# Optimization experiments

Hardware: AMD Instinct MI355X
Metric: run time of the kernel (lower is better)

Reference implementation:

```python
import jax, jax.numpy as jnp
import numpy as np

B, D, H, DH = 2048, 1024, 8, 64  # batch, query_dim, heads, dim_head
INNER = H * DH  # 512


def setup_inputs() -> dict:
    key = jax.random.key(0)
    k0, k1, k2, k3 = jax.random.split(key, 4)
    x = jax.random.normal(k0, (B, D), dtype=jnp.float32)
    Wq = jax.random.normal(k1, (D, INNER), dtype=jnp.float32) * 0.02
    Wkv = jax.random.normal(k2, (D, 2 * INNER), dtype=jnp.float32) * 0.02
    Wout = jax.random.normal(k3, (INNER, D), dtype=jnp.float32) * 0.02
    bout = jnp.zeros((D,), dtype=jnp.float32)
    return {"x": x, "Wq": Wq, "Wkv": Wkv, "Wout": Wout, "bout": bout}


def reference(x, Wq, Wkv, Wout, bout):
    # Faithful to the original: 2D x, attention over the flattened (B*H) axis.
    b = x.shape[0]
    scale = DH ** -0.5
    q = (x @ Wq).reshape(b * H, DH)            # (b h) d
    k, v = jnp.split(x @ Wkv, 2, axis=-1)      # each [b, inner]
    k = k.reshape(b * H, DH)
    v = v.reshape(b * H, DH)
    sim = (q @ k.T) * scale                    # [(b h), (b h)] -- 1 GB intermediate
    attn = jax.nn.softmax(sim, axis=-1)        # dropout_rate = 0 -> identity
    out = (attn @ v).reshape(b, INNER)         # b (h d)
    return out @ Wout + bout                   # project_out path
```

## Files before the change

kernel.cpp:

```cpp
#include <hip/hip_runtime.h>
#include <hip/hip_bf16.h>
#include <stdint.h>


typedef __bf16 bf16_t;
typedef __bf16 bf16x4 __attribute__((ext_vector_type(4)));
typedef __bf16 bf16x8 __attribute__((ext_vector_type(8)));
typedef float floatx4 __attribute__((ext_vector_type(4)));

__device__ __forceinline__ floatx4 mfma16(bf16x8 a, bf16x8 b, floatx4 c) {
    return __builtin_amdgcn_mfma_f32_16x16x32_bf16(a, b, c, 0, 0, 0);
}

__device__ __forceinline__ bf16x8 cvt8(float4 a, float4 b) {
    bf16x8 o;
    o[0] = (bf16_t)a.x; o[1] = (bf16_t)a.y; o[2] = (bf16_t)a.z; o[3] = (bf16_t)a.w;
    o[4] = (bf16_t)b.x; o[5] = (bf16_t)b.y; o[6] = (bf16_t)b.z; o[7] = (bf16_t)b.w;
    return o;
}

__device__ __forceinline__ void transpose_body(const float* __restrict__ in, int N,
                                               bf16_t* __restrict__ out, int ldo,
                                               int bx, int by, int tid, float (*tile)[33]) {
    int n0 = bx * 32, k0 = by * 32;
    int tx = tid & 31, ty = tid >> 5;
#pragma unroll
    for (int i = 0; i < 32; i += 8)
        tile[ty + i][tx] = in[(size_t)(k0 + ty + i) * N + (n0 + tx)];
    __syncthreads();
#pragma unroll
    for (int i = 0; i < 32; i += 8)
        out[(size_t)(n0 + ty + i) * ldo + (k0 + tx)] = (bf16_t)tile[tx][ty + i];
}

__global__ __launch_bounds__(256) void prep_all(const float* __restrict__ x,
                                                bf16_t* __restrict__ xb,
                                                const float* __restrict__ Wq,
                                                const float* __restrict__ Wkv,
                                                const float* __restrict__ Wout,
                                                bf16_t* __restrict__ WtQKV,
                                                bf16_t* __restrict__ WtOut) {
    __shared__ float tile[32][33];
    int b = blockIdx.x, tid = threadIdx.x;
    if (b < 1024) {
        int i = (b * 256 + tid) * 8;
        *(bf16x8*)(xb + i) = cvt8(*(const float4*)(x + i), *(const float4*)(x + i + 4));
    } else if (b < 1536) {
        b -= 1024;
        transpose_body(Wq, 512, WtQKV, 1024, b & 15, b >> 4, tid, tile);
    } else if (b < 2560) {
        b -= 1536;
        transpose_body(Wkv, 1024, WtQKV + 512 * 1024, 1024, b & 31, b >> 5, tid, tile);
    } else {
        b -= 2560;
        transpose_body(Wout, 1024, WtOut, 512, b & 31, b >> 5, tid, tile);
    }
}

template <int OF32, int MI>
__global__ __launch_bounds__(256) void gemm_bt(const bf16_t* __restrict__ A,
                                               const bf16_t* __restrict__ Bt,
                                               const float* __restrict__ bias,
                                               void* __restrict__ Cout,
                                               bf16_t* __restrict__ VtOut, int vt_col0,
                                               int K, int lda, int ldb, int ldc,
                                               float qscale, int qcols) {
    constexpr int MT = MI * 32;
    constexpr int PA = MT / 64;
    constexpr int ABUF = MT * 64;
    __shared__ bf16_t sA[2 * ABUF];
    __shared__ bf16_t sB[2 * 4096];
    int tid = threadIdx.x;
    int wave = tid >> 6, lane = tid & 63;
    int lm = lane & 15, q = lane >> 4;
    int bm = blockIdx.x * MT, bn = blockIdx.y * 64;
    int wm = (wave >> 1) * (MT / 2), wn = (wave & 1) * 32;

    int c0 = (tid & 3) * 2, c1 = c0 + 1;
    int rA[PA], swA[PA];
    size_t srcA0[PA], srcA1[PA];
#pragma unroll
    for (int p = 0; p < PA; ++p) {
        rA[p] = p * 64 + (tid >> 2);
        swA[p] = rA[p] & 7;
        srcA0[p] = (size_t)(bm + rA[p]) * lda + ((c0 ^ swA[p]) << 3);
        srcA1[p] = (size_t)(bm + rA[p]) * lda + ((c1 ^ swA[p]) << 3);
    }
    int rB = tid >> 2, swB = rB & 7;
    size_t srcB0 = (size_t)(bn + rB) * ldb + ((c0 ^ swB) << 3);
    size_t srcB1 = (size_t)(bn + rB) * ldb + ((c1 ^ swB) << 3);

    floatx4 acc[MI][2];
#pragma unroll
    for (int i = 0; i < MI; ++i)
#pragma unroll
        for (int j = 0; j < 2; ++j) acc[i][j] = (floatx4){0.f, 0.f, 0.f, 0.f};

    bf16x8 pa0[PA], pa1[PA], pb0, pb1;
#pragma unroll
    for (int p = 0; p < PA; ++p) {
        pa0[p] = *(const bf16x8*)(A + srcA0[p]);
        pa1[p] = *(const bf16x8*)(A + srcA1[p]);
    }
    pb0 = *(const bf16x8*)(Bt + srcB0);
    pb1 = *(const bf16x8*)(Bt + srcB1);
#pragma unroll
    for (int p = 0; p < PA; ++p) {
        *(bf16x8*)&sA[p * 4096 + tid * 16] = pa0[p];
        *(bf16x8*)&sA[p * 4096 + tid * 16 + 8] = pa1[p];
    }
    *(bf16x8*)&sB[tid * 16] = pb0;
    *(bf16x8*)&sB[tid * 16 + 8] = pb1;
    __syncthreads();

    int po = 0;
    for (int k0 = 0; k0 < K; k0 += 64) {
        int kn = (k0 + 64 < K) ? k0 + 64 : 0;
#pragma unroll
        for (int p = 0; p < PA; ++p) {
            pa0[p] = *(const bf16x8*)(A + srcA0[p] + kn);
            pa1[p] = *(const bf16x8*)(A + srcA1[p] + kn);
        }
        pb0 = *(const bf16x8*)(Bt + srcB0 + kn);
        pb1 = *(const bf16x8*)(Bt + srcB1 + kn);

#pragma unroll
        for (int s = 0; s < 2; ++s) {
            int cs = s * 4 + q;
            bf16x8 af[MI], bfr[2];
#pragma unroll
            for (int i = 0; i < MI; ++i) {
                int row = wm + i * 16 + lm;
                af[i] = *(bf16x8*)&sA[po * ABUF + row * 64 + ((cs ^ (lm & 7)) << 3)];
            }
#pragma unroll
            for (int j = 0; j < 2; ++j) {
                int row = wn + j * 16 + lm;
                bfr[j] = *(bf16x8*)&sB[po * 4096 + row * 64 + ((cs ^ (lm & 7)) << 3)];
            }
#pragma unroll
            for (int i = 0; i < MI; ++i)
#pragma unroll
                for (int j = 0; j < 2; ++j)
                    acc[i][j] = mfma16(af[i], bfr[j], acc[i][j]);
        }

        int qo = po ^ 1;
#pragma unroll
        for (int p = 0; p < PA; ++p) {
            *(bf16x8*)&sA[qo * ABUF + p * 4096 + tid * 16] = pa0[p];
            *(bf16x8*)&sA[qo * ABUF + p * 4096 + tid * 16 + 8] = pa1[p];
        }
        *(bf16x8*)&sB[qo * 4096 + tid * 16] = pb0;
        *(bf16x8*)&sB[qo * 4096 + tid * 16 + 8] = pb1;
        __syncthreads();
        po = qo;
    }

#pragma unroll
    for (int i = 0; i < MI; ++i)
#pragma unroll
        for (int j = 0; j < 2; ++j)
#pragma unroll
            for (int r = 0; r < 4; ++r) {
                int row = bm + wm + i * 16 + q * 4 + r;
                int col = bn + wn + j * 16 + lm;
                float v = acc[i][j][r];
                if (col < qcols) v *= qscale;
                if (bias) v += bias[col];
                if (col >= vt_col0) {
                    int cc = col - vt_col0;
                    VtOut[(size_t)(cc & 63) * 16384 + row * 8 + (cc >> 6)] = (bf16_t)v;
                } else {
                    size_t off = (size_t)row * ldc + col;
                    if (OF32) ((float*)Cout)[off] = v;
                    else      ((bf16_t*)Cout)[off] = (bf16_t)v;
                }
            }
}

__global__ __launch_bounds__(256, 2) void flash_attn(const bf16_t* __restrict__ QK,
                                                     const bf16_t* __restrict__ Vt,
                                                     bf16_t* __restrict__ O,
                                                     float* __restrict__ accP,
                                                     float* __restrict__ lP,
                                                     int kps, int nsplit) {
    __shared__ bf16_t sK[2 * 4096];
    __shared__ bf16_t sVt[2 * 4096];
    int tid = threadIdx.x;
    int wave = tid >> 6, lane = tid & 63;
    int lm = lane & 15, q = lane >> 4;
    int sp = blockIdx.y;
    int qrow0 = blockIdx.x * 256 + wave * 64;

    bf16x8 qf[4][2];
#pragma unroll
    for (int sub = 0; sub < 4; ++sub) {
        int qr = qrow0 + sub * 16 + lm;
        const bf16_t* qp = QK + (size_t)(qr >> 3) * 1024 + (qr & 7) * 64;
        qf[sub][0] = *(const bf16x8*)(qp + q * 8);
        qf[sub][1] = *(const bf16x8*)(qp + 32 + q * 8);
    }

    int sr = tid >> 2;
    int ch0 = (tid & 3) * 2, ch1 = ch0 + 1;
    int swz = sr & 7;
    int lsr = 32 * (sr >> 5) + 8 * ((sr >> 2) & 3) + 4 * ((sr >> 4) & 1) + (sr & 3);
    int ksrcA = (lsr >> 3) * 1024 + (lsr & 7) * 64 + 512 + ((ch0 ^ swz) << 3);
    int ksrcB = (lsr >> 3) * 1024 + (lsr & 7) * 64 + 512 + ((ch1 ^ swz) << 3);
    size_t vsrcA = (size_t)sr * 16384 + ((ch0 ^ swz) << 3);
    size_t vsrcB = (size_t)sr * 16384 + ((ch1 ^ swz) << 3);

    int c0 = q ^ (lm & 7);

    floatx4 acc[4][4];
#pragma unroll
    for (int sub = 0; sub < 4; ++sub)
#pragma unroll
        for (int i = 0; i < 4; ++i) acc[sub][i] = (floatx4){0.f, 0.f, 0.f, 0.f};
    float lacc[4] = {0.f, 0.f, 0.f, 0.f};

    int kt0 = sp * kps, kend = kt0 + kps;

    bf16x8 krA, krB, vrA, vrB;
    {
        const bf16_t* kb = QK + (size_t)kt0 * 128;
        krA = *(const bf16x8*)(kb + ksrcA);
        krB = *(const bf16x8*)(kb + ksrcB);
        vrA = *(const bf16x8*)(Vt + vsrcA + kt0);
        vrB = *(const bf16x8*)(Vt + vsrcB + kt0);
    }
    *(bf16x8*)&sK[tid * 16] = krA; *(bf16x8*)&sK[tid * 16 + 8] = krB;
    *(bf16x8*)&sVt[tid * 16] = vrA; *(bf16x8*)&sVt[tid * 16 + 8] = vrB;
    __syncthreads();

    int po = 0;
    for (int kt = kt0; kt < kend; kt += 64) {
        int ktn = (kt + 64 < kend) ? kt + 64 : kt0;
        const bf16_t* kbn = QK + (size_t)ktn * 128;
        krA = *(const bf16x8*)(kbn + ksrcA);
        krB = *(const bf16x8*)(kbn + ksrcB);
        vrA = *(const bf16x8*)(Vt + vsrcA + ktn);
        vrB = *(const bf16x8*)(Vt + vsrcB + ktn);

        floatx4 s[4][4];
#pragma unroll
        for (int nb = 0; nb < 4; ++nb) {
            int row = po * 4096 + (nb * 16 + lm) * 64;
            bf16x8 k0 = *(bf16x8*)&sK[row + (c0 << 3)];
            bf16x8 k1 = *(bf16x8*)&sK[row + ((c0 ^ 4) << 3)];
#pragma unroll
            for (int sub = 0; sub < 4; ++sub) {
                floatx4 a = (floatx4){0.f, 0.f, 0.f, 0.f};
                a = mfma16(k0, qf[sub][0], a);
                a = mfma16(k1, qf[sub][1], a);
                s[sub][nb] = a;
            }
        }

        bf16x8 pf[4][2];
#pragma unroll
        for (int sub = 0; sub < 4; ++sub) {
#pragma unroll
            for (int nb = 0; nb < 4; ++nb)
#pragma unroll
                for (int r = 0; r < 4; ++r) {
                    float pv = __builtin_amdgcn_exp2f(s[sub][nb][r]);
                    s[sub][nb][r] = pv;
                    lacc[sub] += pv;
                }
#pragma unroll
            for (int jb = 0; jb < 2; ++jb) {
                bf16x8 p;
#pragma unroll
                for (int r = 0; r < 4; ++r) {
                    p[r] = (bf16_t)s[sub][2 * jb][r];
                    p[r + 4] = (bf16_t)s[sub][2 * jb + 1][r];
                }
                pf[sub][jb] = p;
            }
        }

#pragma unroll
        for (int jb = 0; jb < 2; ++jb) {
            bf16x8 av[4];
#pragma unroll
            for (int nd = 0; nd < 4; ++nd)
                av[nd] = *(bf16x8*)&sVt[po * 4096 + (nd * 16 + lm) * 64 +
                                        ((c0 ^ (jb << 2)) << 3)];
#pragma unroll
            for (int sub = 0; sub < 4; ++sub)
#pragma unroll
                for (int nd = 0; nd < 4; ++nd)
                    acc[sub][nd] = mfma16(av[nd], pf[sub][jb], acc[sub][nd]);
        }

        int qo = po ^ 1;
        *(bf16x8*)&sK[qo * 4096 + tid * 16] = krA;
        *(bf16x8*)&sK[qo * 4096 + tid * 16 + 8] = krB;
        *(bf16x8*)&sVt[qo * 4096 + tid * 16] = vrA;
        *(bf16x8*)&sVt[qo * 4096 + tid * 16 + 8] = vrB;
        __syncthreads();
        po = qo;
    }

#pragma unroll
    for (int sub = 0; sub < 4; ++sub) {
        lacc[sub] += __shfl_xor(lacc[sub], 16);
        lacc[sub] += __shfl_xor(lacc[sub], 32);
    }

    if (nsplit == 1) {
#pragma unroll
        for (int sub = 0; sub < 4; ++sub) {
            float inv = 1.f / lacc[sub];
            int row = qrow0 + sub * 16 + lm;
#pragma unroll
            for (int nd = 0; nd < 4; ++nd) {
                bf16x4 o;
#pragma unroll
                for (int r = 0; r < 4; ++r) o[r] = (bf16_t)(acc[sub][nd][r] * inv);
                *(bf16x4*)&O[(size_t)row * 64 + nd * 16 + q * 4] = o;
            }
        }
    } else {
#pragma unroll
        for (int sub = 0; sub < 4; ++sub) {
            int row = qrow0 + sub * 16 + lm;
            size_t base = ((size_t)sp * 16384 + row) * 64;
#pragma unroll
            for (int nd = 0; nd < 4; ++nd) {
                float4 v = {acc[sub][nd][0], acc[sub][nd][1],
                            acc[sub][nd][2], acc[sub][nd][3]};
                *(float4*)&accP[base + nd * 16 + q * 4] = v;
            }
            if (lane < 16) lP[sp * 16384 + row] = lacc[sub];
        }
    }
}

__global__ __launch_bounds__(256) void merge_attn(const float* __restrict__ accP,
                                                  const float* __restrict__ lP,
                                                  bf16_t* __restrict__ O, int nsplit) {
    int idx = blockIdx.x * 256 + threadIdx.x;
    int row = idx >> 4, dh4 = (idx & 15) * 4;
    float4 num = {0.f, 0.f, 0.f, 0.f};
    float den = 0.f;
    for (int s = 0; s < nsplit; ++s) {
        float4 a = *(const float4*)&accP[((size_t)s * 16384 + row) * 64 + dh4];
        num.x += a.x; num.y += a.y; num.z += a.z; num.w += a.w;
        den += lP[s * 16384 + row];
    }
    float inv = 1.f / den;
    bf16x4 o;
    o[0] = (bf16_t)(num.x * inv); o[1] = (bf16_t)(num.y * inv);
    o[2] = (bf16_t)(num.z * inv); o[3] = (bf16_t)(num.w * inv);
    *(bf16x4*)&O[(size_t)row * 64 + dh4] = o;
}

extern "C" void kernel_launch(void* const* d_in, const int* in_sizes, int n_in,
                              void* d_out, int out_size, void* d_ws, size_t ws_size,
                              hipStream_t stream) {
    const float* x    = (const float*)d_in[0];
    const float* Wq   = (const float*)d_in[1];
    const float* Wkv  = (const float*)d_in[2];
    const float* Wout = (const float*)d_in[3];
    const float* bout = (const float*)d_in[4];

    char* ws = (char*)d_ws;
    bf16_t* QK    = (bf16_t*)ws;
    bf16_t* Vt    = (bf16_t*)(ws + 4194304);
    bf16_t* Ob    = (bf16_t*)(ws + 6291456);
    bf16_t* xb    = (bf16_t*)(ws + 8388608);
    bf16_t* WtQKV = (bf16_t*)(ws + 12582912);
    bf16_t* WtOut = (bf16_t*)(ws + 15728640);
    float*  accP  = (float*)(ws + 16777216);

    int nsplit = (ws_size >= (size_t)16777216 + 8 * 4259840) ? 8
               : (ws_size >= (size_t)16777216 + 4 * 4259840) ? 4
               : (ws_size >= (size_t)16777216 + 2 * 4259840) ? 2 : 1;
    float* lP = (float*)(ws + 16777216 + (size_t)nsplit * 4194304);

    prep_all<<<3072, 256, 0, stream>>>(x, xb, Wq, Wkv, Wout, WtQKV, WtOut);

    gemm_bt<0, 2><<<dim3(32, 24), 256, 0, stream>>>(
        xb, WtQKV, nullptr, QK, Vt, 1024, 1024, 1024, 1024, 1024,
        0.18033688011112042f, 512);

    flash_attn<<<dim3(64, nsplit), 256, 0, stream>>>(QK, Vt, Ob, accP, lP,
                                                     16384 / nsplit, nsplit);
    if (nsplit > 1)
        merge_attn<<<1024, 256, 0, stream>>>(accP, lP, Ob, nsplit);

    gemm_bt<1, 2><<<dim3(32, 16), 256, 0, stream>>>(
        Ob, WtOut, bout, d_out, nullptr, 1 << 30, 512, 512, 512, 1024,
        1.0f, 0);
}
```

Baseline: 173.4 us.

## Fuse x fp32-to-bf16 conversion into QKV GEMM and compute softmax row sums via MFMA

The separate fp32-to-bf16 conversion of x is removed from the prep kernel. The QKV GEMM now loads fp32 x directly and converts it while depositing into shared memory, which saves a write and re-read of the bf16 copy but doubles the A-operand global load bytes inside the GEMM. In flash attention, the per-element scalar accumulation of exp values and the final cross-lane shuffles are replaced by an MFMA against a vector of ones. This moves the row-sum work onto the matrix units, at the cost of summing bf16-rounded probabilities instead of fp32 values.

```diff
diff --git a/kernel.cpp b/kernel.cpp
--- a/kernel.cpp
+++ b/kernel.cpp
@@ -33,32 +33,26 @@
         out[(size_t)(n0 + ty + i) * ldo + (k0 + tx)] = (bf16_t)tile[tx][ty + i];
 }
 
-__global__ __launch_bounds__(256) void prep_all(const float* __restrict__ x,
-                                                bf16_t* __restrict__ xb,
-                                                const float* __restrict__ Wq,
+__global__ __launch_bounds__(256) void prep_all(const float* __restrict__ Wq,
                                                 const float* __restrict__ Wkv,
                                                 const float* __restrict__ Wout,
                                                 bf16_t* __restrict__ WtQKV,
                                                 bf16_t* __restrict__ WtOut) {
     __shared__ float tile[32][33];
     int b = blockIdx.x, tid = threadIdx.x;
-    if (b < 1024) {
-        int i = (b * 256 + tid) * 8;
-        *(bf16x8*)(xb + i) = cvt8(*(const float4*)(x + i), *(const float4*)(x + i + 4));
+    if (b < 512) {
+        transpose_body(Wq, 512, WtQKV, 1024, b & 15, b >> 4, tid, tile);
     } else if (b < 1536) {
-        b -= 1024;
-        transpose_body(Wq, 512, WtQKV, 1024, b & 15, b >> 4, tid, tile);
-    } else if (b < 2560) {
-        b -= 1536;
+        b -= 512;
         transpose_body(Wkv, 1024, WtQKV + 512 * 1024, 1024, b & 31, b >> 5, tid, tile);
     } else {
-        b -= 2560;
+        b -= 1536;
         transpose_body(Wout, 1024, WtOut, 512, b & 31, b >> 5, tid, tile);
     }
 }
 
-template <int OF32, int MI>
-__global__ __launch_bounds__(256) void gemm_bt(const bf16_t* __restrict__ A,
+template <int AF32, int OF32, int MI>
+__global__ __launch_bounds__(256) void gemm_bt(const void* __restrict__ Av,
                                                const bf16_t* __restrict__ Bt,
                                                const float* __restrict__ bias,
                                                void* __restrict__ Cout,
@@ -97,30 +91,44 @@
         for (int j = 0; j < 2; ++j) acc[i][j] = (floatx4){0.f, 0.f, 0.f, 0.f};
 
     bf16x8 pa0[PA], pa1[PA], pb0, pb1;
-#pragma unroll
-    for (int p = 0; p < PA; ++p) {
-        pa0[p] = *(const bf16x8*)(A + srcA0[p]);
-        pa1[p] = *(const bf16x8*)(A + srcA1[p]);
-    }
+    float4 fa0[PA][2], fa1[PA][2];
+
+    auto load_a = [&](int kn) {
+#pragma unroll
+        for (int p = 0; p < PA; ++p) {
+            if (AF32) {
+                const float* ap0 = (const float*)Av + srcA0[p] + kn;
+                const float* ap1 = (const float*)Av + srcA1[p] + kn;
+                fa0[p][0] = *(const float4*)ap0; fa0[p][1] = *(const float4*)(ap0 + 4);
+                fa1[p][0] = *(const float4*)ap1; fa1[p][1] = *(const float4*)(ap1 + 4);
+            } else {
+                pa0[p] = *(const bf16x8*)((const bf16_t*)Av + srcA0[p] + kn);
+                pa1[p] = *(const bf16x8*)((const bf16_t*)Av + srcA1[p] + kn);
+            }
+        }
+    };
+    auto deposit = [&](int qo) {
+#pragma unroll
+        for (int p = 0; p < PA; ++p) {
+            bf16x8 v0 = AF32 ? cvt8(fa0[p][0], fa0[p][1]) : pa0[p];
+            bf16x8 v1 = AF32 ? cvt8(fa1[p][0], fa1[p][1]) : pa1[p];
+            *(bf16x8*)&sA[qo * ABUF + p * 4096 + tid * 16] = v0;
+            *(bf16x8*)&sA[qo * ABUF + p * 4096 + tid * 16 + 8] = v1;
+        }
+        *(bf16x8*)&sB[qo * 4096 + tid * 16] = pb0;
+        *(bf16x8*)&sB[qo * 4096 + tid * 16 + 8] = pb1;
+    };
+
+    load_a(0);
     pb0 = *(const bf16x8*)(Bt + srcB0);
     pb1 = *(const bf16x8*)(Bt + srcB1);
-#pragma unroll
-    for (int p = 0; p < PA; ++p) {
-        *(bf16x8*)&sA[p * 4096 + tid * 16] = pa0[p];
-        *(bf16x8*)&sA[p * 4096 + tid * 16 + 8] = pa1[p];
-    }
-    *(bf16x8*)&sB[tid * 16] = pb0;
-    *(bf16x8*)&sB[tid * 16 + 8] = pb1;
+    deposit(0);
     __syncthreads();
 
     int po = 0;
     for (int k0 = 0; k0 < K; k0 += 64) {
         int kn = (k0 + 64 < K) ? k0 + 64 : 0;
-#pragma unroll
-        for (int p = 0; p < PA; ++p) {
-            pa0[p] = *(const bf16x8*)(A + srcA0[p] + kn);
-            pa1[p] = *(const bf16x8*)(A + srcA1[p] + kn);
-        }
+        load_a(kn);
         pb0 = *(const bf16x8*)(Bt + srcB0 + kn);
         pb1 = *(const bf16x8*)(Bt + srcB1 + kn);
 
@@ -146,13 +154,7 @@
         }
 
         int qo = po ^ 1;
-#pragma unroll
-        for (int p = 0; p < PA; ++p) {
-            *(bf16x8*)&sA[qo * ABUF + p * 4096 + tid * 16] = pa0[p];
-            *(bf16x8*)&sA[qo * ABUF + p * 4096 + tid * 16 + 8] = pa1[p];
-        }
-        *(bf16x8*)&sB[qo * 4096 + tid * 16] = pb0;
-        *(bf16x8*)&sB[qo * 4096 + tid * 16 + 8] = pb1;
+        deposit(qo);
         __syncthreads();
         po = qo;
     }
@@ -213,12 +215,18 @@
 
     int c0 = q ^ (lm & 7);
 
+    bf16x8 ones;
+#pragma unroll
+    for (int e = 0; e < 8; ++e) ones[e] = (bf16_t)1.0f;
+
     floatx4 acc[4][4];
 #pragma unroll
     for (int sub = 0; sub < 4; ++sub)
 #pragma unroll
         for (int i = 0; i < 4; ++i) acc[sub][i] = (floatx4){0.f, 0.f, 0.f, 0.f};
-    float lacc[4] = {0.f, 0.f, 0.f, 0.f};
+    floatx4 acc_l[4];
+#pragma unroll
+    for (int sub = 0; sub < 4; ++sub) acc_l[sub] = (floatx4){0.f, 0.f, 0.f, 0.f};
 
     int kt0 = sp * kps, kend = kt0 + kps;
 
@@ -262,22 +270,15 @@
 #pragma unroll
         for (int sub = 0; sub < 4; ++sub) {
 #pragma unroll
-            for (int nb = 0; nb < 4; ++nb)
-#pragma unroll
-                for (int r = 0; r < 4; ++r) {
-                    float pv = __builtin_amdgcn_exp2f(s[sub][nb][r]);
-                    s[sub][nb][r] = pv;
-                    lacc[sub] += pv;
-                }
-#pragma unroll
             for (int jb = 0; jb < 2; ++jb) {
                 bf16x8 p;
 #pragma unroll
                 for (int r = 0; r < 4; ++r) {
-                    p[r] = (bf16_t)s[sub][2 * jb][r];
-                    p[r + 4] = (bf16_t)s[sub][2 * jb + 1][r];
+                    p[r]     = (bf16_t)__builtin_amdgcn_exp2f(s[sub][2 * jb][r]);
+                    p[r + 4] = (bf16_t)__builtin_amdgcn_exp2f(s[sub][2 * jb + 1][r]);
                 }
                 pf[sub][jb] = p;
+                acc_l[sub] = mfma16(ones, p, acc_l[sub]);
             }
         }
 
@@ -304,16 +305,10 @@
         po = qo;
     }
 
-#pragma unroll
-    for (int sub = 0; sub < 4; ++sub) {
-        lacc[sub] += __shfl_xor(lacc[sub], 16);
-        lacc[sub] += __shfl_xor(lacc[sub], 32);
-    }
-
     if (nsplit == 1) {
 #pragma unroll
         for (int sub = 0; sub < 4; ++sub) {
-            float inv = 1.f / lacc[sub];
+            float inv = 1.f / acc_l[sub][0];
             int row = qrow0 + sub * 16 + lm;
 #pragma unroll
             for (int nd = 0; nd < 4; ++nd) {
@@ -334,7 +329,7 @@
                             acc[sub][nd][2], acc[sub][nd][3]};
                 *(float4*)&accP[base + nd * 16 + q * 4] = v;
             }
-            if (lane < 16) lP[sp * 16384 + row] = lacc[sub];
+            if (lane < 16) lP[sp * 16384 + row] = acc_l[sub][0];
         }
     }
 }
@@ -371,20 +366,19 @@
     bf16_t* QK    = (bf16_t*)ws;
     bf16_t* Vt    = (bf16_t*)(ws + 4194304);
     bf16_t* Ob    = (bf16_t*)(ws + 6291456);
-    bf16_t* xb    = (bf16_t*)(ws + 8388608);
-    bf16_t* WtQKV = (bf16_t*)(ws + 12582912);
-    bf16_t* WtOut = (bf16_t*)(ws + 15728640);
-    float*  accP  = (float*)(ws + 16777216);
-
-    int nsplit = (ws_size >= (size_t)16777216 + 8 * 4259840) ? 8
-               : (ws_size >= (size_t)16777216 + 4 * 4259840) ? 4
-               : (ws_size >= (size_t)16777216 + 2 * 4259840) ? 2 : 1;
-    float* lP = (float*)(ws + 16777216 + (size_t)nsplit * 4194304);
-
-    prep_all<<<3072, 256, 0, stream>>>(x, xb, Wq, Wkv, Wout, WtQKV, WtOut);
-
-    gemm_bt<0, 2><<<dim3(32, 24), 256, 0, stream>>>(
-        xb, WtQKV, nullptr, QK, Vt, 1024, 1024, 1024, 1024, 1024,
+    bf16_t* WtQKV = (bf16_t*)(ws + 8388608);
+    bf16_t* WtOut = (bf16_t*)(ws + 11534336);
+    float*  accP  = (float*)(ws + 12582912);
+
+    int nsplit = (ws_size >= (size_t)12582912 + 8 * 4259840) ? 8
+               : (ws_size >= (size_t)12582912 + 4 * 4259840) ? 4
+               : (ws_size >= (size_t)12582912 + 2 * 4259840) ? 2 : 1;
+    float* lP = (float*)(ws + 12582912 + (size_t)nsplit * 4194304);
+
+    prep_all<<<2048, 256, 0, stream>>>(Wq, Wkv, Wout, WtQKV, WtOut);
+
+    gemm_bt<1, 0, 2><<<dim3(32, 24), 256, 0, stream>>>(
+        x, WtQKV, nullptr, QK, Vt, 1024, 1024, 1024, 1024, 1024,
         0.18033688011112042f, 512);
 
     flash_attn<<<dim3(64, nsplit), 256, 0, stream>>>(QK, Vt, Ob, accP, lP,
@@ -392,7 +386,7 @@
     if (nsplit > 1)
         merge_attn<<<1024, 256, 0, stream>>>(accP, lP, Ob, nsplit);
 
-    gemm_bt<1, 2><<<dim3(32, 16), 256, 0, stream>>>(
+    gemm_bt<0, 1, 2><<<dim3(32, 16), 256, 0, stream>>>(
         Ob, WtOut, bout, d_out, nullptr, 1 << 30, 512, 512, 512, 1024,
         1.0f, 0);
 }
```

Result: no change. 173.7 us (+0.1%).
